# Optimization experiments

Measured on AMD Instinct MI355X. Metric: run time of the kernel, lower is better.

## Reference

```python
import jax, jax.numpy as jnp
import numpy as np
from jax import lax

NPOINT = 1024
NSAMPLE = 32
RADIUS = 0.2
EPS = 1e-5  # BatchNorm eps


def _fps(xyz, npoint):
    """Farthest point sampling (deterministic, start at index 0). xyz: (B,N,3) -> idx (B,npoint)."""
    B, N, _ = xyz.shape
    big = jnp.asarray(1e10, xyz.dtype)

    def step(carry, _):
        min_d, last = carry
        cent = xyz[jnp.arange(B), last]                      # (B,3)
        d = jnp.sum((xyz - cent[:, None, :]) ** 2, axis=-1)  # (B,N)
        min_d = jnp.minimum(min_d, d)
        nxt = jnp.argmax(min_d, axis=-1).astype(jnp.int32)
        return (min_d, nxt), last

    init = (jnp.full((B, N), big, xyz.dtype), jnp.zeros((B,), jnp.int32))
    _, idxs = lax.scan(step, init, None, length=npoint)      # (npoint,B)
    return idxs.T                                            # (B,npoint)


def _ball_query(new_xyz, xyz, K, radius):
    """First-K-within-radius neighbors (pytorch3d semantics: pad idx=-1, nn=0)."""
    B, S, _ = new_xyz.shape
    N = xyz.shape[1]
    d2 = jnp.sum((new_xyz[:, :, None, :] - xyz[:, None, :, :]) ** 2, axis=-1)  # (B,S,N)
    mask = d2 < radius * radius
    key = jnp.where(mask, jnp.arange(N, dtype=jnp.int32), jnp.int32(N))
    idx = jnp.sort(key, axis=-1)[..., :K]                    # (B,S,K) first K hits in order
    valid = idx < N
    idx = jnp.where(valid, idx, -1)
    idx_safe = jnp.where(valid, idx, 0)
    g = jnp.take_along_axis(xyz, idx_safe.reshape(B, S * K)[:, :, None], axis=1)
    grouped_xyz = jnp.where(valid[..., None], g.reshape(B, S, K, 3), 0.0)      # padded -> 0
    return idx, grouped_xyz


def _gather_points(points, idx):
    """index_points with torch negative-index semantics (-1 wraps to N-1)."""
    B, N, D = points.shape
    S, K = idx.shape[1], idx.shape[2]
    idx_w = jnp.where(idx < 0, idx + N, idx)
    g = jnp.take_along_axis(points, idx_w.reshape(B, S * K)[:, :, None], axis=1)
    return g.reshape(B, S, K, D)


def _forward(xyz, points, params):
    B, N, C = xyz.shape
    fps_idx = _fps(xyz, NPOINT)                                          # (B,S)
    new_xyz = jnp.take_along_axis(xyz, fps_idx[:, :, None], axis=1)      # (B,S,3)
    idx, grouped_xyz = _ball_query(new_xyz, xyz, NSAMPLE, RADIUS)        # (B,S,K),(B,S,K,3)
    grouped_xyz_norm = grouped_xyz - new_xyz[:, :, None, :]
    grouped_points = _gather_points(points, idx)                         # (B,S,K,D)
    x = jnp.concatenate([grouped_xyz_norm, grouped_points], axis=-1)     # (B,S,K,3+D)
    for (W, b, g, be, m, v) in params:
        x = jnp.einsum('bskc,cd->bskd', x, W) + b                        # 1x1 conv over channels
        x = (x - m) * (g * lax.rsqrt(v + EPS)) + be                      # BN (eval mode)
        x = jax.nn.relu(x)
    new_points = jnp.max(x, axis=2)                                      # max over neighbors -> (B,S,C')
    return new_xyz, new_points


def setup_inputs() -> dict:
    key = jax.random.key(0)
    ks = jax.random.split(key, 32)
    B, N, D = 16, 4096, 64
    mlp = [64, 64, 128]
    inp = {
        'xyz': jax.random.uniform(ks[0], (B, N, 3), jnp.float32),
        'points': jax.random.normal(ks[1], (B, N, D), jnp.float32),
    }
    cin = 3 + D
    k = 2
    for i, cout in enumerate(mlp):
        inp[f'W{i}'] = jax.random.normal(ks[k], (cin, cout), jnp.float32) * (1.0 / np.sqrt(cin)); k += 1
        inp[f'b{i}'] = jax.random.normal(ks[k], (cout,), jnp.float32) * 0.01; k += 1
        inp[f'g{i}'] = jax.random.uniform(ks[k], (cout,), jnp.float32) + 0.5; k += 1
        inp[f'be{i}'] = jax.random.normal(ks[k], (cout,), jnp.float32) * 0.01; k += 1
        inp[f'm{i}'] = jax.random.normal(ks[k], (cout,), jnp.float32) * 0.01; k += 1
        inp[f'v{i}'] = jax.random.uniform(ks[k], (cout,), jnp.float32) + 0.5; k += 1
        cin = cout
    return inp


def reference(xyz, points, W0, b0, g0, be0, m0, v0,
              W1, b1, g1, be1, m1, v1,
              W2, b2, g2, be2, m2, v2):
    params = [(W0, b0, g0, be0, m0, v0),
              (W1, b1, g1, be1, m1, v1),
              (W2, b2, g2, be2, m2, v2)]
    return _forward(xyz, points, params)
```

## Files before the change

kernel.cpp:

```cpp
#include <hip/hip_runtime.h>


typedef unsigned int   u32;
typedef unsigned long long u64;

#define NB 16
#define NP 4096
#define NS 1024
#define NK 32
#define NITEM (NB * NS / 2)

#define DPP_UPD(v, ctrl) ((u32)__builtin_amdgcn_update_dpp((int)(v), (int)(v), (ctrl), 0xf, 0xf, false))
#define U64_STEP(v, ctrl) { \
  u32 _lo = DPP_UPD((u32)(v), ctrl); \
  u32 _hi = DPP_UPD((u32)((v) >> 32), ctrl); \
  u64 _o = (((u64)_hi) << 32) | _lo; \
  v = (v > _o) ? v : _o; }
#define WAVE_RED_U64MAX(v) do { U64_STEP(v,0x111); U64_STEP(v,0x112); U64_STEP(v,0x114); \
                                U64_STEP(v,0x118); U64_STEP(v,0x142); U64_STEP(v,0x143); } while (0)
#define UMAX_DPP(v, ctrl) { u32 _o = DPP_UPD(v, ctrl); v = (v > _o) ? v : _o; }
#define HALF_RED_UMAX32(v) do { UMAX_DPP(v,0x111); UMAX_DPP(v,0x112); UMAX_DPP(v,0x114); \
                                UMAX_DPP(v,0x118); UMAX_DPP(v,0x142); } while (0)

struct FpsS { float4 pt[NP]; u64 red[2][4]; };
struct HalfS {
  float x0[64 * 67];
  u64 masks[2][64];
  int offs[2][64];
  int idx_ls[2][NK];
  float cent[8];
};
struct ConS { HalfS h[2]; float sAB[512]; int shi; };
union SMem { FpsS f; ConS c; };

__device__ __forceinline__ float dload_f(const float* p) {
  return __uint_as_float(__hip_atomic_load((const u32*)p, __ATOMIC_RELAXED, __HIP_MEMORY_SCOPE_AGENT));
}

__global__ void __launch_bounds__(512)
fused_kernel(const float* __restrict__ xyz, const float* __restrict__ pts,
             const float* __restrict__ W0, const float* __restrict__ b0, const float* __restrict__ g0,
             const float* __restrict__ be0, const float* __restrict__ m0, const float* __restrict__ v0,
             const float* __restrict__ W1, const float* __restrict__ b1, const float* __restrict__ g1,
             const float* __restrict__ be1, const float* __restrict__ m1, const float* __restrict__ v1,
             const float* __restrict__ W2, const float* __restrict__ b2, const float* __restrict__ g2,
             const float* __restrict__ be2, const float* __restrict__ m2, const float* __restrict__ v2,
             float* __restrict__ out0, float* __restrict__ out1,
             int* __restrict__ progress, int* __restrict__ ctr)
{
  __shared__ SMem sm;
  const int t = threadIdx.x;

  if (blockIdx.x < NB) {
    asm volatile("s_setprio 3");
    FpsS& S = sm.f;
    const int b = blockIdx.x;
    const int lane = t & 63, wv = t >> 6;
    const float* bx = xyz + (size_t)b * NP * 3;
    for (int i = t; i < NP; i += 512) {
      S.pt[i] = make_float4(bx[i * 3 + 0], bx[i * 3 + 1], bx[i * 3 + 2], 0.0f);
    }
    __syncthreads();
    if (wv >= 4) return;

    float px[16], py[16], pz[16], md[16];
#pragma unroll
    for (int p = 0; p < 16; ++p) {
      float4 f4 = S.pt[p * 256 + t];
      px[p] = f4.x; py[p] = f4.y; pz[p] = f4.z;
      md[p] = 1e10f;
    }
    const u32 nt = ~(u32)t;
    float4 c4 = S.pt[0];
    float cx = c4.x, cy = c4.y, cz = c4.z;
    float hx = cx, hy = cy, hz = cz;

    for (int it = 1; it < NS; ++it) {
      u32 vb, ca;
      {
        float dx = __fsub_rn(px[0], cx);
        float dy = __fsub_rn(py[0], cy);
        float dz = __fsub_rn(pz[0], cz);
        float d  = __fadd_rn(__fadd_rn(__fmul_rn(dx, dx), __fmul_rn(dy, dy)), __fmul_rn(dz, dz));
        float m2 = fminf(md[0], d);
        md[0] = m2;
        vb = __float_as_uint(m2);
        ca = nt;
      }
#pragma unroll
      for (int p = 1; p < 16; ++p) {
        float dx = __fsub_rn(px[p], cx);
        float dy = __fsub_rn(py[p], cy);
        float dz = __fsub_rn(pz[p], cz);
        float d  = __fadd_rn(__fadd_rn(__fmul_rn(dx, dx), __fmul_rn(dy, dy)), __fmul_rn(dz, dz));
        float m2 = fminf(md[p], d);
        md[p] = m2;
        u32 mb = __float_as_uint(m2);
        bool gt = mb > vb;
        vb = gt ? mb : vb;
        ca = gt ? (nt - (u32)(p * 256)) : ca;
      }
      u64 key = (((u64)vb) << 32) | ca;
      WAVE_RED_U64MAX(key);
      const int par = it & 1;
      if (lane == 63) S.red[par][wv] = key;
      __syncthreads();
      const ulonglong2* rp2 = (const ulonglong2*)S.red[par];
      ulonglong2 kk0 = rp2[0], kk1 = rp2[1];
      u64 m01 = (kk0.x > kk0.y) ? kk0.x : kk0.y;
      u64 m23 = (kk1.x > kk1.y) ? kk1.x : kk1.y;
      u64 bk = (m01 > m23) ? m01 : m23;
      const int idx = (int)(~(u32)bk);
      float4 cc = S.pt[idx];
      cx = cc.x; cy = cc.y; cz = cc.z;
      if (wv == 0) {
        bool cap = (lane == (it & 15));
        hx = cap ? cx : hx;
        hy = cap ? cy : hy;
        hz = cap ? cz : hz;
        if ((it & 15) == 15) {
          if (lane < 16) {
            float* o = out0 + ((size_t)b * NS + (it - 15) + lane) * 3;
            o[0] = hx; o[1] = hy; o[2] = hz;
          }
          if (lane == 0)
            __hip_atomic_store(&progress[b * 16], it + 1, __ATOMIC_RELEASE, __HIP_MEMORY_SCOPE_AGENT);
        }
      }
    }
    return;
  }

  ConS& C = sm.c;
  const int half = t >> 8;
  const int u = t & 255;
  const int lane = t & 63;
  const int hw = u >> 6;
  HalfS& H = C.h[half];
  const float R2 = (float)(0.2 * 0.2);

  if (t < 256) {
    const float *gp, *bep, *mp, *vp, *bpp; int c, base, bcoff;
    if (t < 64)       { c = t;       gp = g0; bep = be0; mp = m0; vp = v0; bpp = b0; base = 0;   bcoff = 64;  }
    else if (t < 128) { c = t - 64;  gp = g1; bep = be1; mp = m1; vp = v1; bpp = b1; base = 128; bcoff = 64;  }
    else              { c = t - 128; gp = g2; bep = be2; mp = m2; vp = v2; bpp = b2; base = 256; bcoff = 128; }
    float a = gp[c] / sqrtf(vp[c] + 1e-5f);
    C.sAB[base + c] = a;
    C.sAB[base + bcoff + c] = (bpp[c] - mp[c]) * a + bep[c];
  }
  __syncthreads();

  for (;;) {
    if (t == 0) C.shi = atomicAdd(ctr, 2);
    __syncthreads();
    const int i0 = C.shi;
    if (i0 >= NITEM) break;
    const int item = i0 + half;
    const bool active = item < NITEM;
    const int b = item & 15, pr = item >> 4, s0 = pr * 2;

    if (u == 0 && active) {
      const int need = s0 + 2;
      while (__hip_atomic_load(&progress[b * 16], __ATOMIC_ACQUIRE, __HIP_MEMORY_SCOPE_AGENT) < need)
        __builtin_amdgcn_s_sleep(32);
      const float* cp = out0 + ((size_t)b * NS + s0) * 3;
#pragma unroll
      for (int i2 = 0; i2 < 6; ++i2) H.cent[i2] = dload_f(cp + i2);
    }
    __syncthreads();
    const float c0x = H.cent[0], c0y = H.cent[1], c0z = H.cent[2];
    const float c1x = H.cent[3], c1y = H.cent[4], c1z = H.cent[5];
    const float* bx = xyz + (size_t)b * NP * 3;

    if (active) {
      for (int c = 0; c < 16; ++c) {
        int ch = hw * 16 + c;
        int i = ch * 64 + lane;
        float X = bx[i * 3 + 0], Y = bx[i * 3 + 1], Z = bx[i * 3 + 2];
        float dx0 = __fsub_rn(c0x, X), dy0 = __fsub_rn(c0y, Y), dz0 = __fsub_rn(c0z, Z);
        float d20 = __fadd_rn(__fadd_rn(__fmul_rn(dx0, dx0), __fmul_rn(dy0, dy0)), __fmul_rn(dz0, dz0));
        u64 mA = __ballot(d20 < R2);
        float dx1 = __fsub_rn(c1x, X), dy1 = __fsub_rn(c1y, Y), dz1 = __fsub_rn(c1z, Z);
        float d21 = __fadd_rn(__fadd_rn(__fmul_rn(dx1, dx1), __fmul_rn(dy1, dy1)), __fmul_rn(dz1, dz1));
        u64 mB = __ballot(d21 < R2);
        if (lane == 0) { H.masks[0][ch] = mA; H.masks[1][ch] = mB; }
      }
      if (u < 64) H.idx_ls[u >> 5][u & 31] = -1;
    }
    __syncthreads();
    if (active && (hw & 1) == 0) {
      int cent = hw >> 1;
      int cnt = __popcll(H.masks[cent][lane]);
      int inc = cnt;
#pragma unroll
      for (int off = 1; off < 64; off <<= 1) {
        int n = __shfl_up(inc, off);
        if (lane >= off) inc += n;
      }
      H.offs[cent][lane] = inc - cnt;
    }
    __syncthreads();
    if (active) {
      for (int c = 0; c < 16; ++c) {
        int ch = hw * 16 + c;
#pragma unroll
        for (int cent = 0; cent < 2; ++cent) {
          int base = H.offs[cent][ch];
          if (base >= NK) continue;
          u64 m = H.masks[cent][ch];
          if ((m >> lane) & 1ull) {
            int slot = base + __popcll(m & ((1ull << lane) - 1ull));
            if (slot < NK) H.idx_ls[cent][slot] = ch * 64 + lane;
          }
        }
      }
    }
    __syncthreads();
    if (active) {
      int cent = u >> 7, tt = u & 127;
      int row = tt >> 2, q = tt & 3;
      int id = H.idx_ls[cent][row];
      int prow = (id < 0) ? (NP - 1) : id;
      const float4* p4 = (const float4*)(pts + ((size_t)b * NP + prow) * 64 + q * 16);
      float4 va = p4[0], vb = p4[1], vc = p4[2], vd = p4[3];
      float* dst = &H.x0[(cent * 32 + row) * 67 + 3 + q * 16];
      dst[0]  = va.x; dst[1]  = va.y; dst[2]  = va.z; dst[3]  = va.w;
      dst[4]  = vb.x; dst[5]  = vb.y; dst[6]  = vb.z; dst[7]  = vb.w;
      dst[8]  = vc.x; dst[9]  = vc.y; dst[10] = vc.z; dst[11] = vc.w;
      dst[12] = vd.x; dst[13] = vd.y; dst[14] = vd.z; dst[15] = vd.w;
      if (u < 64) {
        int c2 = u >> 5, slot = u & 31;
        int id2 = H.idx_ls[c2][slot];
        float ax = c2 ? c1x : c0x, ay = c2 ? c1y : c0y, az = c2 ? c1z : c0z;
        float gx, gy, gz;
        if (id2 >= 0) {
          gx = __fsub_rn(bx[id2 * 3 + 0], ax);
          gy = __fsub_rn(bx[id2 * 3 + 1], ay);
          gz = __fsub_rn(bx[id2 * 3 + 2], az);
        } else {
          gx = 0.0f - ax; gy = 0.0f - ay; gz = 0.0f - az;
        }
        float* d2p = &H.x0[(c2 * 32 + slot) * 67];
        d2p[0] = gx; d2p[1] = gy; d2p[2] = gz;
      }
    }
    __syncthreads();

    const int j0 = __builtin_amdgcn_readfirstlane(hw * 16);
    {
      float acc[16];
#pragma unroll
      for (int i = 0; i < 16; ++i) acc[i] = 0.0f;
      if (active) {
        const float* xr = &H.x0[lane * 67];
#pragma unroll 2
        for (int c = 0; c < 67; ++c) {
          float xv = xr[c];
          const float4* wr = (const float4*)(W0 + c * 64 + j0);
          float4 wa = wr[0], wb = wr[1], wc = wr[2], wd = wr[3];
          acc[0]  = fmaf(xv, wa.x, acc[0]);  acc[1]  = fmaf(xv, wa.y, acc[1]);
          acc[2]  = fmaf(xv, wa.z, acc[2]);  acc[3]  = fmaf(xv, wa.w, acc[3]);
          acc[4]  = fmaf(xv, wb.x, acc[4]);  acc[5]  = fmaf(xv, wb.y, acc[5]);
          acc[6]  = fmaf(xv, wb.z, acc[6]);  acc[7]  = fmaf(xv, wb.w, acc[7]);
          acc[8]  = fmaf(xv, wc.x, acc[8]);  acc[9]  = fmaf(xv, wc.y, acc[9]);
          acc[10] = fmaf(xv, wc.z, acc[10]); acc[11] = fmaf(xv, wc.w, acc[11]);
          acc[12] = fmaf(xv, wd.x, acc[12]); acc[13] = fmaf(xv, wd.y, acc[13]);
          acc[14] = fmaf(xv, wd.z, acc[14]); acc[15] = fmaf(xv, wd.w, acc[15]);
        }
      }
      __syncthreads();
      if (active) {
#pragma unroll
        for (int i = 0; i < 16; ++i) {
          float y = fmaf(acc[i], C.sAB[j0 + i], C.sAB[64 + j0 + i]);
          H.x0[lane * 67 + j0 + i] = fmaxf(y, 0.0f);
        }
      }
    }
    __syncthreads();
    {
      float acc[16];
#pragma unroll
      for (int i = 0; i < 16; ++i) acc[i] = 0.0f;
      if (active) {
        const float* xr = &H.x0[lane * 67];
#pragma unroll 2
        for (int c = 0; c < 64; ++c) {
          float xv = xr[c];
          const float4* wr = (const float4*)(W1 + c * 64 + j0);
          float4 wa = wr[0], wb = wr[1], wc = wr[2], wd = wr[3];
          acc[0]  = fmaf(xv, wa.x, acc[0]);  acc[1]  = fmaf(xv, wa.y, acc[1]);
          acc[2]  = fmaf(xv, wa.z, acc[2]);  acc[3]  = fmaf(xv, wa.w, acc[3]);
          acc[4]  = fmaf(xv, wb.x, acc[4]);  acc[5]  = fmaf(xv, wb.y, acc[5]);
          acc[6]  = fmaf(xv, wb.z, acc[6]);  acc[7]  = fmaf(xv, wb.w, acc[7]);
          acc[8]  = fmaf(xv, wc.x, acc[8]);  acc[9]  = fmaf(xv, wc.y, acc[9]);
          acc[10] = fmaf(xv, wc.z, acc[10]); acc[11] = fmaf(xv, wc.w, acc[11]);
          acc[12] = fmaf(xv, wd.x, acc[12]); acc[13] = fmaf(xv, wd.y, acc[13]);
          acc[14] = fmaf(xv, wd.z, acc[14]); acc[15] = fmaf(xv, wd.w, acc[15]);
        }
      }
      __syncthreads();
      if (active) {
#pragma unroll
        for (int i = 0; i < 16; ++i) {
          float y = fmaf(acc[i], C.sAB[128 + j0 + i], C.sAB[192 + j0 + i]);
          H.x0[lane * 67 + j0 + i] = fmaxf(y, 0.0f);
        }
      }
    }
    __syncthreads();
    if (active) {
      const int j3 = __builtin_amdgcn_readfirstlane(hw * 32);
      float acc[32];
#pragma unroll
      for (int i = 0; i < 32; ++i) acc[i] = 0.0f;
      const float* xr = &H.x0[lane * 67];
      for (int c = 0; c < 64; ++c) {
        float xv = xr[c];
        const float4* wr = (const float4*)(W2 + c * 128 + j3);
#pragma unroll
        for (int q = 0; q < 8; ++q) {
          float4 wq = wr[q];
          acc[q * 4 + 0] = fmaf(xv, wq.x, acc[q * 4 + 0]);
          acc[q * 4 + 1] = fmaf(xv, wq.y, acc[q * 4 + 1]);
          acc[q * 4 + 2] = fmaf(xv, wq.z, acc[q * 4 + 2]);
          acc[q * 4 + 3] = fmaf(xv, wq.w, acc[q * 4 + 3]);
        }
      }
#pragma unroll
      for (int i = 0; i < 32; ++i) {
        float y = fmaf(acc[i], C.sAB[256 + j3 + i], C.sAB[384 + j3 + i]);
        u32 mb = __float_as_uint(fmaxf(y, 0.0f));
        HALF_RED_UMAX32(mb);
        acc[i] = __uint_as_float(mb);
      }
      if (lane == 31 || lane == 63) {
        int cent = lane >> 5;
        float4* op = (float4*)(out1 + ((size_t)b * NS + s0 + cent) * 128 + j3);
#pragma unroll
        for (int q = 0; q < 8; ++q)
          op[q] = make_float4(acc[q * 4 + 0], acc[q * 4 + 1], acc[q * 4 + 2], acc[q * 4 + 3]);
      }
    }
  }
}

extern "C" void kernel_launch(void* const* d_in, const int* in_sizes, int n_in,
                              void* d_out, int out_size, void* d_ws, size_t ws_size,
                              hipStream_t stream) {
  const float* xyz = (const float*)d_in[0];
  const float* pts = (const float*)d_in[1];
  const float* W0 = (const float*)d_in[2];  const float* b0 = (const float*)d_in[3];
  const float* g0 = (const float*)d_in[4];  const float* be0 = (const float*)d_in[5];
  const float* m0 = (const float*)d_in[6];  const float* v0 = (const float*)d_in[7];
  const float* W1 = (const float*)d_in[8];  const float* b1 = (const float*)d_in[9];
  const float* g1 = (const float*)d_in[10]; const float* be1 = (const float*)d_in[11];
  const float* m1 = (const float*)d_in[12]; const float* v1 = (const float*)d_in[13];
  const float* W2 = (const float*)d_in[14]; const float* b2 = (const float*)d_in[15];
  const float* g2 = (const float*)d_in[16]; const float* be2 = (const float*)d_in[17];
  const float* m2 = (const float*)d_in[18]; const float* v2 = (const float*)d_in[19];

  float* out0 = (float*)d_out;
  float* out1 = out0 + NB * NS * 3;
  int* prog = (int*)d_ws;
  int* ctr  = (int*)d_ws + 320;

  hipMemsetAsync(d_ws, 0, 2048, stream);

  fused_kernel<<<256, 512, 0, stream>>>(
      xyz, pts,
      W0, b0, g0, be0, m0, v0,
      W1, b1, g1, be1, m1, v1,
      W2, b2, g2, be2, m2, v2,
      out0, out1, prog, ctr);
}
```

Baseline: 770.7 us.

## Spread FPS over 8 waves with 8 points per thread and tree-reduced keys

The farthest-point-sampling blocks now keep all 8 waves active instead of 4, so each thread holds 8 points rather than 16. The per-thread argmax becomes a tree of packed 64-bit key comparisons instead of a serial compare chain, and the cross-wave reduction reads 8 partial results. This shortens the serial per-iteration critical path of the 1024-step FPS loop. The cost is a barrier across more waves and a wider final reduction.

```diff
diff --git a/kernel.cpp b/kernel.cpp
--- a/kernel.cpp
+++ b/kernel.cpp
@@ -22,7 +22,7 @@
 #define HALF_RED_UMAX32(v) do { UMAX_DPP(v,0x111); UMAX_DPP(v,0x112); UMAX_DPP(v,0x114); \
                                 UMAX_DPP(v,0x118); UMAX_DPP(v,0x142); } while (0)
 
-struct FpsS { float4 pt[NP]; u64 red[2][4]; };
+struct FpsS { float4 pt[NP]; u64 red[2][8]; };
 struct HalfS {
   float x0[64 * 67];
   u64 masks[2][64];
@@ -61,12 +61,11 @@
       S.pt[i] = make_float4(bx[i * 3 + 0], bx[i * 3 + 1], bx[i * 3 + 2], 0.0f);
     }
     __syncthreads();
-    if (wv >= 4) return;
-
-    float px[16], py[16], pz[16], md[16];
-#pragma unroll
-    for (int p = 0; p < 16; ++p) {
-      float4 f4 = S.pt[p * 256 + t];
+
+    float px[8], py[8], pz[8], md[8];
+#pragma unroll
+    for (int p = 0; p < 8; ++p) {
+      float4 f4 = S.pt[p * 512 + t];
       px[p] = f4.x; py[p] = f4.y; pz[p] = f4.z;
       md[p] = 1e10f;
     }
@@ -76,40 +75,41 @@
     float hx = cx, hy = cy, hz = cz;
 
     for (int it = 1; it < NS; ++it) {
-      u32 vb, ca;
-      {
-        float dx = __fsub_rn(px[0], cx);
-        float dy = __fsub_rn(py[0], cy);
-        float dz = __fsub_rn(pz[0], cz);
-        float d  = __fadd_rn(__fadd_rn(__fmul_rn(dx, dx), __fmul_rn(dy, dy)), __fmul_rn(dz, dz));
-        float m2 = fminf(md[0], d);
-        md[0] = m2;
-        vb = __float_as_uint(m2);
-        ca = nt;
-      }
-#pragma unroll
-      for (int p = 1; p < 16; ++p) {
+      float d2[8];
+#pragma unroll
+      for (int p = 0; p < 8; ++p) {
         float dx = __fsub_rn(px[p], cx);
         float dy = __fsub_rn(py[p], cy);
         float dz = __fsub_rn(pz[p], cz);
-        float d  = __fadd_rn(__fadd_rn(__fmul_rn(dx, dx), __fmul_rn(dy, dy)), __fmul_rn(dz, dz));
-        float m2 = fminf(md[p], d);
+        d2[p] = __fadd_rn(__fadd_rn(__fmul_rn(dx, dx), __fmul_rn(dy, dy)), __fmul_rn(dz, dz));
+      }
+      u64 kk[8];
+#pragma unroll
+      for (int p = 0; p < 8; ++p) {
+        float m2 = fminf(md[p], d2[p]);
         md[p] = m2;
-        u32 mb = __float_as_uint(m2);
-        bool gt = mb > vb;
-        vb = gt ? mb : vb;
-        ca = gt ? (nt - (u32)(p * 256)) : ca;
-      }
-      u64 key = (((u64)vb) << 32) | ca;
+        kk[p] = (((u64)__float_as_uint(m2)) << 32) | (u32)(nt - (u32)(p * 512));
+      }
+      u64 a0 = (kk[0] > kk[1]) ? kk[0] : kk[1];
+      u64 a1 = (kk[2] > kk[3]) ? kk[2] : kk[3];
+      u64 a2 = (kk[4] > kk[5]) ? kk[4] : kk[5];
+      u64 a3 = (kk[6] > kk[7]) ? kk[6] : kk[7];
+      u64 b0_ = (a0 > a1) ? a0 : a1;
+      u64 b1_ = (a2 > a3) ? a2 : a3;
+      u64 key = (b0_ > b1_) ? b0_ : b1_;
       WAVE_RED_U64MAX(key);
       const int par = it & 1;
       if (lane == 63) S.red[par][wv] = key;
       __syncthreads();
       const ulonglong2* rp2 = (const ulonglong2*)S.red[par];
-      ulonglong2 kk0 = rp2[0], kk1 = rp2[1];
-      u64 m01 = (kk0.x > kk0.y) ? kk0.x : kk0.y;
-      u64 m23 = (kk1.x > kk1.y) ? kk1.x : kk1.y;
-      u64 bk = (m01 > m23) ? m01 : m23;
+      ulonglong2 q0 = rp2[0], q1 = rp2[1], q2 = rp2[2], q3 = rp2[3];
+      u64 e0 = (q0.x > q0.y) ? q0.x : q0.y;
+      u64 e1 = (q1.x > q1.y) ? q1.x : q1.y;
+      u64 e2 = (q2.x > q2.y) ? q2.x : q2.y;
+      u64 e3 = (q3.x > q3.y) ? q3.x : q3.y;
+      u64 f0 = (e0 > e1) ? e0 : e1;
+      u64 f1 = (e2 > e3) ? e2 : e3;
+      u64 bk = (f0 > f1) ? f0 : f1;
       const int idx = (int)(~(u32)bk);
       float4 cc = S.pt[idx];
       cx = cc.x; cy = cc.y; cz = cc.z;
```

New measurement: 807.3 us. 1.05x slower.
